# Kernel optimization log

Hardware: AMD Instinct MI355X
Metric: run time of the kernel (lower is better)

Reference implementation:

```python
import jax, jax.numpy as jnp
import numpy as np

B = 8000      # graphs in batch
D = 128       # input_dim
H = 128       # hidden_dim
COUNTS = (2 + (np.arange(B) % 125)).astype(np.int32)   # nodes per graph in [2,126], sum = 512000
N = int(COUNTS.sum())
SEG = np.repeat(np.arange(B, dtype=np.int32), COUNTS)  # sorted graph id per node


def setup_inputs() -> dict:
    key = jax.random.key(0)
    k1, k2, k3, k4, k5 = jax.random.split(key, 5)
    return {
        "feats": jax.random.normal(k1, (N, D), dtype=jnp.float32),
        "W_u": jax.random.normal(k2, (D, H), dtype=jnp.float32) * 0.1,
        "W_v": jax.random.normal(k3, (D, H), dtype=jnp.float32) * 0.1,
        "b_v": jax.random.normal(k4, (H,), dtype=jnp.float32) * 0.1,
        "w_e": jax.random.normal(k5, (H, 1), dtype=jnp.float32) * 0.1,
        "seg": jnp.asarray(SEG),
        "counts": jnp.asarray(COUNTS),
    }


def reference(feats, W_u, W_v, b_v, w_e, seg, counts):
    nseg = counts.shape[0]
    fdt = feats.dtype
    # per-graph mean and max(|.|) over nodes, stacked interleaved as in the torch
    # code: rows of the table are [mean_g0, max_g0, mean_g1, max_g1, ...]
    ssum = jax.ops.segment_sum(feats, seg, num_segments=nseg, indices_are_sorted=True)
    mean = ssum / counts.astype(fdt)[:, None]                       # [B, D]
    mx = jax.ops.segment_max(jnp.abs(feats), seg, num_segments=nseg,
                             indices_are_sorted=True)               # [B, D]
    table = jnp.stack([mean, mx], axis=1).reshape(2 * nseg, -1)     # [2B, D]
    feat_u = feats @ W_u                                            # [N, H]
    # torch indexes the (2B)-row interleaved table with graph ids in [0,B)
    feat_v = (table @ W_v + b_v)[seg]                               # [N, H]
    e = jax.nn.sigmoid(feat_u + feat_v) @ w_e                       # [N, 1]
    # my_segment: exp only where nonzero, then segment-normalize (segment softmax)
    ee = jnp.where(e != 0, jnp.exp(e), e)
    den = jax.ops.segment_sum(ee, seg, num_segments=nseg, indices_are_sorted=True)[seg]
    alpha = ee / den                                                # [N, 1]
    # attention-weighted segment-sum pooling
    rst = jax.ops.segment_sum(feats * alpha, seg, num_segments=nseg,
                              indices_are_sorted=True)              # [B, D]
    return rst[:, None, :]                                          # [B, order=1, D]
```

## Files before the change

### kernel.cpp

```cpp
#include <hip/hip_runtime.h>
#include <hip/hip_bf16.h>
#include <math.h>

#define DD 128

typedef __attribute__((ext_vector_type(8))) short bf16x8;
typedef __attribute__((ext_vector_type(4))) float f32x4;

static __device__ __forceinline__ short f2bf(float x) {
    union { float f; unsigned u; } v; v.f = x;
    unsigned r = v.u + 0x7FFFu + ((v.u >> 16) & 1u);
    return (short)(r >> 16);
}

__global__ void k0_combined(const int* __restrict__ counts, int* __restrict__ offs, int B,
                            const float* __restrict__ Wu, short* __restrict__ wuT)
{
    if (blockIdx.x == 0) {
        __shared__ int part[256];
        int t = threadIdx.x;
        int chunk = (B + 255) >> 8;
        int s = 0;
        for (int i = 0; i < chunk; ++i) {
            int idx = t * chunk + i;
            if (idx < B) s += counts[idx];
        }
        part[t] = s;
        __syncthreads();
        for (int off = 1; off < 256; off <<= 1) {
            int val = (t >= off) ? part[t - off] : 0;
            __syncthreads();
            part[t] += val;
            __syncthreads();
        }
        int run = (t > 0) ? part[t - 1] : 0;
        for (int i = 0; i < chunk; ++i) {
            int idx = t * chunk + i;
            if (idx < B) { offs[idx] = run; run += counts[idx]; }
        }
    } else {
        int idx = (blockIdx.x - 1) * 256 + threadIdx.x;
        int h = idx >> 7, k = idx & 127;
        wuT[(size_t)h * DD + k] = f2bf(Wu[(size_t)k * DD + h]);
    }
}

__global__ __launch_bounds__(256)
void k1_stats(const float* __restrict__ feats, const int* __restrict__ offs,
              const int* __restrict__ counts, float* __restrict__ mean,
              float* __restrict__ amax)
{
    int g = blockIdx.x;
    int s = offs[g], c = counts[g];
    int t = threadIdx.x;
    int col = (t & 31) * 4;
    int r0 = t >> 5;
    float4 sm = {0.f, 0.f, 0.f, 0.f};
    float4 mx = {0.f, 0.f, 0.f, 0.f};
    const float* base = feats + (size_t)s * DD + col;
    #pragma unroll 4
    for (int i = r0; i < c; i += 8) {
        float4 v = *(const float4*)(base + (size_t)i * DD);
        sm.x += v.x; sm.y += v.y; sm.z += v.z; sm.w += v.w;
        mx.x = fmaxf(mx.x, fabsf(v.x)); mx.y = fmaxf(mx.y, fabsf(v.y));
        mx.z = fmaxf(mx.z, fabsf(v.z)); mx.w = fmaxf(mx.w, fabsf(v.w));
    }
    __shared__ float ls[8][DD];
    __shared__ float lm[8][DD];
    *(float4*)&ls[r0][col] = sm;
    *(float4*)&lm[r0][col] = mx;
    __syncthreads();
    if (t < DD) {
        float ss = 0.f, mm = 0.f;
        #pragma unroll
        for (int r = 0; r < 8; ++r) {
            ss += ls[r][t];
            mm = fmaxf(mm, lm[r][t]);
        }
        mean[(size_t)g * DD + t] = ss / (float)c;
        amax[(size_t)g * DD + t] = mm;
    }
}

__global__ __launch_bounds__(128)
void k2_vtab(const float* __restrict__ mean, const float* __restrict__ amax,
             const float* __restrict__ Wv, const float* __restrict__ bv,
             float* __restrict__ vtab, int B)
{
    __shared__ float rows[16][DD];
    int g0 = blockIdx.x * 16;
    int h = threadIdx.x;
    for (int i = 0; i < 16; ++i) {
        int g = g0 + i;
        float val = 0.f;
        if (g < B) {
            int gg = g >> 1;
            const float* src = (g & 1) ? &amax[(size_t)gg * DD] : &mean[(size_t)gg * DD];
            val = src[h];
        }
        rows[i][h] = val;
    }
    __syncthreads();
    float acc[16];
    float bvh = bv[h];
    #pragma unroll
    for (int i = 0; i < 16; ++i) acc[i] = bvh;
    for (int d = 0; d < DD; d += 2) {
        float w0 = Wv[(size_t)d * DD + h];
        float w1 = Wv[(size_t)(d + 1) * DD + h];
        #pragma unroll
        for (int i = 0; i < 16; ++i) {
            float2 r = *(const float2*)&rows[i][d];
            acc[i] = fmaf(r.x, w0, acc[i]);
            acc[i] = fmaf(r.y, w1, acc[i]);
        }
    }
    #pragma unroll
    for (int i = 0; i < 16; ++i) {
        int g = g0 + i;
        if (g < B) vtab[(size_t)g * DD + h] = acc[i];
    }
}

__global__ __launch_bounds__(256)
void kb_fused(const float* __restrict__ feats, const short* __restrict__ wuT,
              const float* __restrict__ vtab, const float* __restrict__ we,
              const int* __restrict__ offs, const int* __restrict__ counts,
              float* __restrict__ out)
{
    __shared__ float eel[128];
    __shared__ float pool[4][DD];
    __shared__ float dparts[4];

    const int g = blockIdx.x;
    const int s = offs[g], c = counts[g];
    const int t = threadIdx.x;
    const int w = t >> 6, lane = t & 63;
    const int l15 = lane & 15, kg = lane >> 4;

    const int tb0 = w * 16;
    const int tb1 = (w + 4) * 16;
    const int nact = (tb1 < c) ? 2 : ((tb0 < c) ? 1 : 0);

    f32x4 acc[2][8];
    #pragma unroll
    for (int nt = 0; nt < 2; ++nt)
        #pragma unroll
        for (int ht = 0; ht < 8; ++ht)
            acc[nt][ht] = (f32x4){0.f, 0.f, 0.f, 0.f};

    if (nact > 0) {
        int r0 = tb0 + l15; r0 = (r0 < c) ? r0 : (c - 1);
        int r1 = tb1 + l15; r1 = (r1 < c) ? r1 : (c - 1);
        const float* a0p = feats + (size_t)(s + r0) * DD;
        const float* a1p = feats + (size_t)(s + r1) * DD;
        const short* bp = wuT + (size_t)l15 * DD + kg * 8;

        #pragma unroll
        for (int ks = 0; ks < 4; ++ks) {
            const int ko = ks * 32 + kg * 8;
            bf16x8 fa[2];
            {
                float4 x0 = *(const float4*)(a0p + ko);
                float4 x1 = *(const float4*)(a0p + ko + 4);
                union { bf16x8 v; short sh[8]; } u;
                u.sh[0] = f2bf(x0.x); u.sh[1] = f2bf(x0.y); u.sh[2] = f2bf(x0.z); u.sh[3] = f2bf(x0.w);
                u.sh[4] = f2bf(x1.x); u.sh[5] = f2bf(x1.y); u.sh[6] = f2bf(x1.z); u.sh[7] = f2bf(x1.w);
                fa[0] = u.v;
            }
            if (nact > 1) {
                float4 x0 = *(const float4*)(a1p + ko);
                float4 x1 = *(const float4*)(a1p + ko + 4);
                union { bf16x8 v; short sh[8]; } u;
                u.sh[0] = f2bf(x0.x); u.sh[1] = f2bf(x0.y); u.sh[2] = f2bf(x0.z); u.sh[3] = f2bf(x0.w);
                u.sh[4] = f2bf(x1.x); u.sh[5] = f2bf(x1.y); u.sh[6] = f2bf(x1.z); u.sh[7] = f2bf(x1.w);
                fa[1] = u.v;
            }
            bf16x8 bf[8];
            #pragma unroll
            for (int ht = 0; ht < 8; ++ht)
                bf[ht] = *(const bf16x8*)(bp + (size_t)(ht * 16) * DD + ks * 32);
            #pragma unroll
            for (int ht = 0; ht < 8; ++ht) {
                acc[0][ht] = __builtin_amdgcn_mfma_f32_16x16x32_bf16(fa[0], bf[ht], acc[0][ht], 0, 0, 0);
                if (nact > 1)
                    acc[1][ht] = __builtin_amdgcn_mfma_f32_16x16x32_bf16(fa[1], bf[ht], acc[1][ht], 0, 0, 0);
            }
        }

        float wv[8], vgv[8];
        #pragma unroll
        for (int ht = 0; ht < 8; ++ht) {
            wv[ht]  = we[l15 + ht * 16];
            vgv[ht] = vtab[(size_t)g * DD + l15 + ht * 16];
        }
        #pragma unroll
        for (int nt = 0; nt < 2; ++nt) {
            if (nt < nact) {
                const int tb = (nt == 0) ? tb0 : tb1;
                #pragma unroll
                for (int r = 0; r < 4; ++r) {
                    int node = tb + kg * 4 + r;
                    float p = 0.f;
                    #pragma unroll
                    for (int ht = 0; ht < 8; ++ht) {
                        float x = acc[nt][ht][r] + vgv[ht];
                        float sg = 1.f / (1.f + __expf(-x));
                        p = fmaf(sg, wv[ht], p);
                    }
                    p += __shfl_xor(p, 1);
                    p += __shfl_xor(p, 2);
                    p += __shfl_xor(p, 4);
                    p += __shfl_xor(p, 8);
                    if (l15 == 0 && node < c)
                        eel[node] = (p != 0.f) ? __expf(p) : p;
                }
            }
        }
    }
    __syncthreads();

    {
        float2 pl = {0.f, 0.f};
        float dw = 0.f;
        const float* base = feats + (size_t)s * DD + lane * 2;
        #pragma unroll 4
        for (int i = w; i < c; i += 4) {
            float wi = eel[i];
            float2 v = *(const float2*)(base + (size_t)i * DD);
            dw += wi;
            pl.x = fmaf(v.x, wi, pl.x);
            pl.y = fmaf(v.y, wi, pl.y);
        }
        pool[w][lane * 2]     = pl.x;
        pool[w][lane * 2 + 1] = pl.y;
        if (lane == 0) dparts[w] = dw;
    }
    __syncthreads();

    if (t < DD) {
        float den = (dparts[0] + dparts[1]) + (dparts[2] + dparts[3]);
        float acc2 = ((pool[0][t] + pool[1][t]) + (pool[2][t] + pool[3][t]));
        out[(size_t)g * DD + t] = acc2 / den;
    }
}

extern "C" void kernel_launch(void* const* d_in, const int* in_sizes, int n_in,
                              void* d_out, int out_size, void* d_ws, size_t ws_size,
                              hipStream_t stream)
{
    const float* feats  = (const float*)d_in[0];
    const float* Wu     = (const float*)d_in[1];
    const float* Wv     = (const float*)d_in[2];
    const float* bv     = (const float*)d_in[3];
    const float* we     = (const float*)d_in[4];
    const int*   counts = (const int*)d_in[6];
    const int B = in_sizes[6];

    char* w = (char*)d_ws;
    int*   offs = (int*)w;    w += ((size_t)B * sizeof(int) + 255) & ~(size_t)255;
    float* mean = (float*)w;  w += (size_t)B * DD * sizeof(float);
    float* amax = (float*)w;  w += (size_t)B * DD * sizeof(float);
    float* vtab = (float*)w;  w += (size_t)B * DD * sizeof(float);
    short* wuT  = (short*)w;  w += (size_t)DD * DD * sizeof(short);

    k0_combined<<<65, 256, 0, stream>>>(counts, offs, B, Wu, wuT);
    k1_stats<<<B, 256, 0, stream>>>(feats, offs, counts, mean, amax);
    k2_vtab<<<(B + 15) / 16, 128, 0, stream>>>(mean, amax, Wv, bv, vtab, B);
    kb_fused<<<B, 256, 0, stream>>>(feats, wuT, vtab, we, offs, counts, (float*)d_out);
}
```

Measured before the change: 281.8 us.

## Stage graph features as bf16 in swizzled LDS and reuse them for pooling

The fused kernel now loads each graph's node features once, converts them to bf16, and writes them into a 32KB XOR-swizzled shared-memory tile. Both the MFMA projection and the attention-weighted pooling read from that tile, so feats is no longer read from global memory a second time. The cost is that pooling now runs on bf16-rounded features, which loses accuracy. The 32KB of LDS per block also limits occupancy; launch bounds now request 4 blocks.

```diff
diff --git a/kernel.cpp b/kernel.cpp
--- a/kernel.cpp
+++ b/kernel.cpp
@@ -11,6 +11,10 @@
     union { float f; unsigned u; } v; v.f = x;
     unsigned r = v.u + 0x7FFFu + ((v.u >> 16) & 1u);
     return (short)(r >> 16);
+}
+static __device__ __forceinline__ float bf2f(unsigned short h) {
+    union { unsigned u; float f; } v; v.u = ((unsigned)h) << 16;
+    return v.f;
 }
 
 __global__ void k0_combined(const int* __restrict__ counts, int* __restrict__ offs, int B,
@@ -122,14 +126,15 @@
     }
 }
 
-__global__ __launch_bounds__(256)
+__global__ __launch_bounds__(256, 4)
 void kb_fused(const float* __restrict__ feats, const short* __restrict__ wuT,
               const float* __restrict__ vtab, const float* __restrict__ we,
               const int* __restrict__ offs, const int* __restrict__ counts,
               float* __restrict__ out)
 {
+    __shared__ short fe[128 * 128];
     __shared__ float eel[128];
-    __shared__ float pool[4][DD];
+    __shared__ float red[4][DD];
     __shared__ float dparts[4];
 
     const int g = blockIdx.x;
@@ -137,111 +142,94 @@
     const int t = threadIdx.x;
     const int w = t >> 6, lane = t & 63;
     const int l15 = lane & 15, kg = lane >> 4;
-
-    const int tb0 = w * 16;
-    const int tb1 = (w + 4) * 16;
-    const int nact = (tb1 < c) ? 2 : ((tb0 < c) ? 1 : 0);
-
-    f32x4 acc[2][8];
-    #pragma unroll
-    for (int nt = 0; nt < 2; ++nt)
-        #pragma unroll
-        for (int ht = 0; ht < 8; ++ht)
-            acc[nt][ht] = (f32x4){0.f, 0.f, 0.f, 0.f};
-
-    if (nact > 0) {
-        int r0 = tb0 + l15; r0 = (r0 < c) ? r0 : (c - 1);
-        int r1 = tb1 + l15; r1 = (r1 < c) ? r1 : (c - 1);
-        const float* a0p = feats + (size_t)(s + r0) * DD;
-        const float* a1p = feats + (size_t)(s + r1) * DD;
-        const short* bp = wuT + (size_t)l15 * DD + kg * 8;
-
-        #pragma unroll
-        for (int ks = 0; ks < 4; ++ks) {
-            const int ko = ks * 32 + kg * 8;
-            bf16x8 fa[2];
-            {
-                float4 x0 = *(const float4*)(a0p + ko);
-                float4 x1 = *(const float4*)(a0p + ko + 4);
-                union { bf16x8 v; short sh[8]; } u;
-                u.sh[0] = f2bf(x0.x); u.sh[1] = f2bf(x0.y); u.sh[2] = f2bf(x0.z); u.sh[3] = f2bf(x0.w);
-                u.sh[4] = f2bf(x1.x); u.sh[5] = f2bf(x1.y); u.sh[6] = f2bf(x1.z); u.sh[7] = f2bf(x1.w);
-                fa[0] = u.v;
-            }
-            if (nact > 1) {
-                float4 x0 = *(const float4*)(a1p + ko);
-                float4 x1 = *(const float4*)(a1p + ko + 4);
-                union { bf16x8 v; short sh[8]; } u;
-                u.sh[0] = f2bf(x0.x); u.sh[1] = f2bf(x0.y); u.sh[2] = f2bf(x0.z); u.sh[3] = f2bf(x0.w);
-                u.sh[4] = f2bf(x1.x); u.sh[5] = f2bf(x1.y); u.sh[6] = f2bf(x1.z); u.sh[7] = f2bf(x1.w);
-                fa[1] = u.v;
-            }
-            bf16x8 bf[8];
-            #pragma unroll
-            for (int ht = 0; ht < 8; ++ht)
-                bf[ht] = *(const bf16x8*)(bp + (size_t)(ht * 16) * DD + ks * 32);
-            #pragma unroll
-            for (int ht = 0; ht < 8; ++ht) {
-                acc[0][ht] = __builtin_amdgcn_mfma_f32_16x16x32_bf16(fa[0], bf[ht], acc[0][ht], 0, 0, 0);
-                if (nact > 1)
-                    acc[1][ht] = __builtin_amdgcn_mfma_f32_16x16x32_bf16(fa[1], bf[ht], acc[1][ht], 0, 0, 0);
-            }
-        }
-
-        float wv[8], vgv[8];
-        #pragma unroll
-        for (int ht = 0; ht < 8; ++ht) {
-            wv[ht]  = we[l15 + ht * 16];
-            vgv[ht] = vtab[(size_t)g * DD + l15 + ht * 16];
-        }
-        #pragma unroll
-        for (int nt = 0; nt < 2; ++nt) {
-            if (nt < nact) {
-                const int tb = (nt == 0) ? tb0 : tb1;
+    char* feb = (char*)fe;
+
+    const int cpad = (c + 15) & ~15;
+    const int nch = cpad * 16;
+    #pragma unroll 2
+    for (int ch = t; ch < nch; ch += 256) {
+        int row = ch >> 4, sub = ch & 15;
+        union { bf16x8 v; short sh[8]; } u;
+        if (row < c) {
+            const float4* gp = (const float4*)(feats + (size_t)(s + row) * DD + sub * 8);
+            float4 a = gp[0], b = gp[1];
+            u.sh[0] = f2bf(a.x); u.sh[1] = f2bf(a.y); u.sh[2] = f2bf(a.z); u.sh[3] = f2bf(a.w);
+            u.sh[4] = f2bf(b.x); u.sh[5] = f2bf(b.y); u.sh[6] = f2bf(b.z); u.sh[7] = f2bf(b.w);
+        } else {
+            u.v = (bf16x8){0, 0, 0, 0, 0, 0, 0, 0};
+        }
+        *(bf16x8*)(feb + row * 256 + ((sub * 16) ^ ((row & 7) << 4))) = u.v;
+    }
+    __syncthreads();
+
+    float wv[8], vgv[8];
+    #pragma unroll
+    for (int ht = 0; ht < 8; ++ht) {
+        wv[ht]  = we[l15 + ht * 16];
+        vgv[ht] = vtab[(size_t)g * DD + l15 + ht * 16];
+    }
+
+    #pragma unroll
+    for (int p = 0; p < 2; ++p) {
+        const int tb = (w + p * 4) * 16;
+        if (tb < c) {
+            bf16x8 af[4];
+            #pragma unroll
+            for (int ks = 0; ks < 4; ++ks)
+                af[ks] = *(const bf16x8*)(feb + (tb + l15) * 256 +
+                                          ((ks * 64 + kg * 16) ^ ((l15 & 7) << 4)));
+            f32x4 acc[8];
+            #pragma unroll
+            for (int ht = 0; ht < 8; ++ht) acc[ht] = (f32x4){0.f, 0.f, 0.f, 0.f};
+            #pragma unroll
+            for (int ks = 0; ks < 4; ++ks) {
                 #pragma unroll
-                for (int r = 0; r < 4; ++r) {
-                    int node = tb + kg * 4 + r;
-                    float p = 0.f;
-                    #pragma unroll
-                    for (int ht = 0; ht < 8; ++ht) {
-                        float x = acc[nt][ht][r] + vgv[ht];
-                        float sg = 1.f / (1.f + __expf(-x));
-                        p = fmaf(sg, wv[ht], p);
-                    }
-                    p += __shfl_xor(p, 1);
-                    p += __shfl_xor(p, 2);
-                    p += __shfl_xor(p, 4);
-                    p += __shfl_xor(p, 8);
-                    if (l15 == 0 && node < c)
-                        eel[node] = (p != 0.f) ? __expf(p) : p;
+                for (int ht = 0; ht < 8; ++ht) {
+                    bf16x8 bfr = *(const bf16x8*)(wuT + (size_t)(l15 + ht * 16) * DD + ks * 32 + kg * 8);
+                    acc[ht] = __builtin_amdgcn_mfma_f32_16x16x32_bf16(af[ks], bfr, acc[ht], 0, 0, 0);
                 }
             }
+            #pragma unroll
+            for (int r = 0; r < 4; ++r) {
+                int node = tb + kg * 4 + r;
+                float pp = 0.f;
+                #pragma unroll
+                for (int ht = 0; ht < 8; ++ht) {
+                    float x = acc[ht][r] + vgv[ht];
+                    float sg = 1.f / (1.f + __expf(-x));
+                    pp = fmaf(sg, wv[ht], pp);
+                }
+                pp += __shfl_xor(pp, 1);
+                pp += __shfl_xor(pp, 2);
+                pp += __shfl_xor(pp, 4);
+                pp += __shfl_xor(pp, 8);
+                if (l15 == 0 && node < c)
+                    eel[node] = (pp != 0.f) ? __expf(pp) : pp;
+            }
         }
     }
     __syncthreads();
 
     {
-        float2 pl = {0.f, 0.f};
-        float dw = 0.f;
-        const float* base = feats + (size_t)s * DD + lane * 2;
+        float px = 0.f, py = 0.f, dw = 0.f;
         #pragma unroll 4
         for (int i = w; i < c; i += 4) {
+            unsigned pv = *(const unsigned*)(feb + i * 256 + ((lane * 4) ^ ((i & 7) << 4)));
             float wi = eel[i];
-            float2 v = *(const float2*)(base + (size_t)i * DD);
             dw += wi;
-            pl.x = fmaf(v.x, wi, pl.x);
-            pl.y = fmaf(v.y, wi, pl.y);
-        }
-        pool[w][lane * 2]     = pl.x;
-        pool[w][lane * 2 + 1] = pl.y;
+            px = fmaf(bf2f((unsigned short)(pv & 0xffffu)), wi, px);
+            py = fmaf(bf2f((unsigned short)(pv >> 16)), wi, py);
+        }
+        red[w][lane * 2]     = px;
+        red[w][lane * 2 + 1] = py;
         if (lane == 0) dparts[w] = dw;
     }
     __syncthreads();
 
     if (t < DD) {
         float den = (dparts[0] + dparts[1]) + (dparts[2] + dparts[3]);
-        float acc2 = ((pool[0][t] + pool[1][t]) + (pool[2][t] + pool[3][t]));
-        out[(size_t)g * DD + t] = acc2 / den;
+        float a2 = (red[0][t] + red[1][t]) + (red[2][t] + red[3][t]);
+        out[(size_t)g * DD + t] = a2 / den;
     }
 }
 
```

After: 250.3 us. 11.2% less time.
